# Kernel optimization log

Measured on AMD Instinct MI355X. Metric: run time of the kernel, lower is better.

The kernel has to match this reference:

```python
import jax, jax.numpy as jnp
import numpy as np

B, N, D, NS, H, ITERS = 16, 2048, 128, 8, 128, 3
EPS = 1e-8


def _ln(x, g, b):
    m = jnp.mean(x, -1, keepdims=True)
    v = jnp.mean((x - m) ** 2, -1, keepdims=True)
    return (x - m) * jax.lax.rsqrt(v + 1e-5) * g + b


def _gru(x, h, Wih, Whh, bih, bhh):
    # PyTorch GRUCell math
    gi = x @ Wih.T + bih
    gh = h @ Whh.T + bhh
    ir, iz, inn = jnp.split(gi, 3, -1)
    hr, hz, hn = jnp.split(gh, 3, -1)
    r = jax.nn.sigmoid(ir + hr)
    z = jax.nn.sigmoid(iz + hz)
    n = jnp.tanh(inn + r * hn)
    return (1.0 - z) * n + z * h


def setup_inputs() -> dict:
    key = jax.random.key(0)
    ks = jax.random.split(key, 16)

    def lin(k, out_d, in_d):
        lim = 1.0 / np.sqrt(in_d)
        return jax.random.uniform(k, (out_d, in_d), jnp.float32, -lim, lim)

    return {
        "inputs": jax.random.normal(ks[0], (B, N, D), jnp.float32),
        "init_noise": jax.random.normal(ks[1], (B, NS, 2 * D), jnp.float32),
        "slots_mu": jax.random.normal(ks[2], (1, 1, 2 * D), jnp.float32),
        "slots_logsigma": jax.random.normal(ks[3], (1, 1, 2 * D), jnp.float32) * 0.08,  # ~xavier scale
        "Wq": lin(ks[4], D, D),
        "Wk": lin(ks[5], D, D),
        "gru_Wih": lin(ks[6], 3 * D, D),
        "gru_Whh": lin(ks[7], 3 * D, D),
        "gru_bih": jnp.zeros((3 * D,), jnp.float32),
        "gru_bhh": jnp.zeros((3 * D,), jnp.float32),
        "mlp_mu_W1": lin(ks[8], H, D),
        "mlp_mu_b1": jnp.zeros((H,), jnp.float32),
        "mlp_mu_W2": lin(ks[9], D, H),
        "mlp_mu_b2": jnp.zeros((D,), jnp.float32),
        "ln_in_g": jnp.ones((D,), jnp.float32),
        "ln_in_b": jnp.zeros((D,), jnp.float32),
        "ln_slots_g": jnp.ones((2 * D,), jnp.float32),
        "ln_slots_b": jnp.zeros((2 * D,), jnp.float32),
        "ln_mu_g": jnp.ones((D,), jnp.float32),
        "ln_mu_b": jnp.zeros((D,), jnp.float32),
        "mlp_out_W1": lin(ks[10], 2 * H, 2 * D),
        "mlp_out_b1": jnp.zeros((2 * H,), jnp.float32),
        "mlp_out_W2": lin(ks[11], D, 2 * H),
        "mlp_out_b2": jnp.zeros((D,), jnp.float32),
    }


def _forward(inputs, init_noise, slots_mu, slots_logsigma, Wq, Wk,
             gru_Wih, gru_Whh, gru_bih, gru_bhh,
             mlp_mu_W1, mlp_mu_b1, mlp_mu_W2, mlp_mu_b2,
             ln_in_g, ln_in_b, ln_slots_g, ln_slots_b, ln_mu_g, ln_mu_b,
             mlp_out_W1, mlp_out_b1, mlp_out_W2, mlp_out_b2):
    x = _ln(inputs, ln_in_g, ln_in_b)                      # (B,N,D)
    k = x @ Wk.T
    v = k                                                  # original uses to_k for both k and v
    slots = slots_mu + jnp.exp(slots_logsigma) * init_noise  # (B,NS,2D)
    pi_cl = jnp.full((B, NS, 1), 1.0 / NS, inputs.dtype)

    def step(slots, pi_cl):
        s = _ln(slots, ln_slots_g, ln_slots_b)
        mu_s, ls_s = jnp.split(s, 2, -1)                   # (B,NS,D) each
        q_mu = mu_s @ Wq.T
        q_ls = ls_s @ Wq.T
        inv_var = jnp.exp(-2.0 * q_ls)                     # 1 / exp(q_logsigma)^2
        diff = k[:, None, :, :] - q_mu[:, :, None, :]      # (B,NS,N,D)
        dots = jnp.einsum('bind,bid->bin', diff * diff, inv_var)
        dots_exp = (jnp.exp(-dots) + EPS) * pi_cl          # (B,NS,N)
        gammas = dots_exp / dots_exp.sum(1, keepdims=True)
        attn = gammas / gammas.sum(-1, keepdims=True)
        upd = jnp.einsum('bjd,bij->bid', v, attn)          # (B,NS,D)
        upd = _gru(upd.reshape(-1, D), mu_s.reshape(-1, D),
                   gru_Wih, gru_Whh, gru_bih, gru_bhh).reshape(B, NS, D)
        h = _ln(upd, ln_mu_g, ln_mu_b)
        upd = upd + (jax.nn.relu(h @ mlp_mu_W1.T + mlp_mu_b1) @ mlp_mu_W2.T + mlp_mu_b2)
        diff2 = v[:, None, :, :] - upd[:, :, None, :]      # (B,NS,N,D)
        upd_ls = 0.5 * jnp.log(jnp.einsum('bind,bin->bid', diff2 * diff2 + EPS, attn))
        slots_new = jnp.concatenate([upd, upd_ls], -1)
        pi_new = gammas.sum(-1, keepdims=True)
        pi_new = pi_new / pi_new.shape[2]                  # shape[2]==1: faithful no-op from original
        return slots_new, pi_new

    for _ in range(ITERS):
        slots, pi_cl = step(slots, pi_cl)
    slots, pi_cl = step(jax.lax.stop_gradient(slots), pi_cl)
    h = jax.nn.relu(slots @ mlp_out_W1.T + mlp_out_b1)
    return h @ mlp_out_W2.T + mlp_out_b2                   # (B,NS,D)


def reference(inputs, init_noise, slots_mu, slots_logsigma, Wq, Wk,
              gru_Wih, gru_Whh, gru_bih, gru_bhh,
              mlp_mu_W1, mlp_mu_b1, mlp_mu_W2, mlp_mu_b2,
              ln_in_g, ln_in_b, ln_slots_g, ln_slots_b, ln_mu_g, ln_mu_b,
              mlp_out_W1, mlp_out_b1, mlp_out_W2, mlp_out_b2):
    return _forward(inputs, init_noise, slots_mu, slots_logsigma, Wq, Wk,
                    gru_Wih, gru_Whh, gru_bih, gru_bhh,
                    mlp_mu_W1, mlp_mu_b1, mlp_mu_W2, mlp_mu_b2,
                    ln_in_g, ln_in_b, ln_slots_g, ln_slots_b, ln_mu_g, ln_mu_b,
                    mlp_out_W1, mlp_out_b1, mlp_out_W2, mlp_out_b2)
```

## Files before the change

kernel.cpp:

```cpp
#include <hip/hip_runtime.h>

#define EPS_ 1e-8f

constexpr int OFF_K     = 0;
constexpr int OFF_WQT   = 4194304;
constexpr int OFF_WKT   = OFF_WQT  + 16384;
constexpr int OFF_WIHT  = OFF_WKT  + 16384;
constexpr int OFF_WHHT  = OFF_WIHT + 49152;
constexpr int OFF_WM1T  = OFF_WHHT + 49152;
constexpr int OFF_WM2T  = OFF_WM1T + 16384;
constexpr int OFF_WO1T  = OFF_WM2T + 16384;
constexpr int OFF_WO2T  = OFF_WO1T + 65536;
constexpr int OFF_SLOTS = OFF_WO2T + 32768;
constexpr int OFF_PI    = OFF_SLOTS+ 32768;
constexpr int OFF_MUS   = OFF_PI   + 128;
constexpr int OFF_WA    = OFF_MUS  + 16384;
constexpr int OFF_WB    = OFF_WA   + 16384;
constexpr int OFF_UN    = OFF_WB   + 16384;
constexpr int OFF_S2    = OFF_UN   + 524288;
constexpr int OFF_DEN   = OFF_S2   + 524288;
constexpr int OFF_CZ    = OFF_DEN  + 4096;

__global__ __launch_bounds__(256) void init_kernel(
    const float* __restrict__ Wq,  const float* __restrict__ Wk,
    const float* __restrict__ Wih, const float* __restrict__ Whh,
    const float* __restrict__ Wm1, const float* __restrict__ Wm2,
    const float* __restrict__ Wo1, const float* __restrict__ Wo2,
    const float* __restrict__ smu, const float* __restrict__ sls,
    const float* __restrict__ noise, float* __restrict__ ws) {
  int idx = blockIdx.x * 256 + threadIdx.x;
  if (idx < 16384) { int j = idx >> 7, d = idx & 127; ws[OFF_WQT + d*128 + j] = Wq[idx]; return; }
  idx -= 16384;
  if (idx < 16384) { int j = idx >> 7, d = idx & 127; ws[OFF_WKT + d*128 + j] = Wk[idx]; return; }
  idx -= 16384;
  if (idx < 49152) { int j = idx >> 7, d = idx & 127; ws[OFF_WIHT + d*384 + j] = Wih[idx]; return; }
  idx -= 49152;
  if (idx < 49152) { int j = idx >> 7, d = idx & 127; ws[OFF_WHHT + d*384 + j] = Whh[idx]; return; }
  idx -= 49152;
  if (idx < 16384) { int j = idx >> 7, d = idx & 127; ws[OFF_WM1T + d*128 + j] = Wm1[idx]; return; }
  idx -= 16384;
  if (idx < 16384) { int j = idx >> 7, d = idx & 127; ws[OFF_WM2T + d*128 + j] = Wm2[idx]; return; }
  idx -= 16384;
  if (idx < 65536) { int j = idx >> 8, d = idx & 255; ws[OFF_WO1T + d*256 + j] = Wo1[idx]; return; }
  idx -= 65536;
  if (idx < 32768) { int j = idx >> 8, m = idx & 255; ws[OFF_WO2T + m*128 + j] = Wo2[idx]; return; }
  idx -= 32768;
  if (idx < 32768) { int c = idx & 255; ws[OFF_SLOTS + idx] = smu[c] + expf(sls[c]) * noise[idx]; return; }
  idx -= 32768;
  if (idx < 128) { ws[OFF_PI + idx] = 0.125f; }
}

__global__ __launch_bounds__(256) void k_kernel(
    const float* __restrict__ xin, const float* __restrict__ g, const float* __restrict__ bb,
    const float* __restrict__ WkT, float* __restrict__ kout) {
  __shared__ float xsT[128][32];
  __shared__ float2 red[32][8];
  __shared__ float mrow[32], srow[32];
  int t = threadIdx.x;
  long long base = (long long)blockIdx.x * 32 * 128;
  int row = t >> 3, cg = t & 7;
  const float4* src = (const float4*)(xin + base + row * 128 + cg * 16);
  float4 v0 = src[0], v1 = src[1], v2 = src[2], v3 = src[3];
  const float4* g4p = (const float4*)(g + cg * 16);
  const float4* b4p = (const float4*)(bb + cg * 16);
  float4 g0 = g4p[0], g1 = g4p[1], g2 = g4p[2], g3 = g4p[3];
  float4 bv0 = b4p[0], bv1 = b4p[1], bv2 = b4p[2], bv3 = b4p[3];
  float vals[16];
  *(float4*)&vals[0]  = v0; *(float4*)&vals[4]  = v1;
  *(float4*)&vals[8]  = v2; *(float4*)&vals[12] = v3;
  float gl[16], bl[16];
  *(float4*)&gl[0] = g0; *(float4*)&gl[4] = g1; *(float4*)&gl[8] = g2; *(float4*)&gl[12] = g3;
  *(float4*)&bl[0] = bv0; *(float4*)&bl[4] = bv1; *(float4*)&bl[8] = bv2; *(float4*)&bl[12] = bv3;
  {
    float s = 0.f, ss = 0.f;
    #pragma unroll
    for (int i = 0; i < 16; ++i) { float v = vals[i]; s += v; ss = fmaf(v, v, ss); }
    red[row][cg] = make_float2(s, ss);
  }
  __syncthreads();
  if (t < 32) {
    float s = 0.f, ss = 0.f;
    #pragma unroll
    for (int c = 0; c < 8; ++c) { float2 p = red[t][c]; s += p.x; ss += p.y; }
    float m = s * (1.0f / 128.0f);
    float var = ss * (1.0f / 128.0f) - m * m;
    mrow[t] = m; srow[t] = rsqrtf(var + 1e-5f);
  }
  __syncthreads();
  {
    float m = mrow[row], is = srow[row];
    #pragma unroll
    for (int i = 0; i < 16; ++i) {
      int d = cg * 16 + i;
      int rs = row ^ (((d >> 2) & 7) << 2);
      xsT[d][rs] = (vals[i] - m) * is * gl[i] + bl[i];
    }
  }
  __syncthreads();
  int j = t & 127, rh = t >> 7;
  int r0 = rh * 16;
  float acc[16];
  #pragma unroll
  for (int i = 0; i < 16; ++i) acc[i] = 0.f;
  #pragma unroll 4
  for (int d = 0; d < 128; ++d) {
    float wv = WkT[d * 128 + j];
    int X = ((d >> 2) & 7) << 2;
    #pragma unroll
    for (int gi = 0; gi < 4; ++gi) {
      int off = (r0 + gi * 4) ^ X;
      float4 xv = *(const float4*)&xsT[d][off];
      acc[gi * 4 + 0] = fmaf(xv.x, wv, acc[gi * 4 + 0]);
      acc[gi * 4 + 1] = fmaf(xv.y, wv, acc[gi * 4 + 1]);
      acc[gi * 4 + 2] = fmaf(xv.z, wv, acc[gi * 4 + 2]);
      acc[gi * 4 + 3] = fmaf(xv.w, wv, acc[gi * 4 + 3]);
    }
  }
  #pragma unroll
  for (int i = 0; i < 16; ++i) kout[base + (long long)(r0 + i) * 128 + j] = acc[i];
}

__global__ __launch_bounds__(256) void s1_kernel(
    const float* __restrict__ slots, const float* __restrict__ g, const float* __restrict__ bb,
    const float* __restrict__ WqT, float* __restrict__ mus,
    float* __restrict__ wA, float* __restrict__ wB, float* __restrict__ cz) {
  __shared__ float sl[256];
  __shared__ float2 wr[4];
  __shared__ float qs_l[128], ivs_l[128];
  __shared__ float wrC[4];
  int t = threadIdx.x, bi = blockIdx.x;
  float v = slots[bi * 256 + t];
  float s = v, ss = v * v;
  #pragma unroll
  for (int o = 32; o > 0; o >>= 1) { s += __shfl_down(s, o); ss += __shfl_down(ss, o); }
  if ((t & 63) == 0) wr[t >> 6] = make_float2(s, ss);
  __syncthreads();
  float fs  = wr[0].x + wr[1].x + wr[2].x + wr[3].x;
  float fss = wr[0].y + wr[1].y + wr[2].y + wr[3].y;
  float m   = fs * (1.0f/256.0f);
  float var = fss * (1.0f/256.0f) - m * m;
  float isr = rsqrtf(var + 1e-5f);
  float sn  = (v - m) * isr * g[t] + bb[t];
  sl[t] = sn;
  __syncthreads();
  if (t < 128) {
    float acc = 0.f;
    #pragma unroll 4
    for (int d = 0; d < 128; ++d) acc = fmaf(sl[d], WqT[d * 128 + t], acc);
    qs_l[t] = acc;
    mus[bi * 128 + t] = sn;
  } else {
    int jj = t - 128;
    float acc = 0.f;
    #pragma unroll 4
    for (int d = 0; d < 128; ++d) acc = fmaf(sl[128 + d], WqT[d * 128 + jj], acc);
    ivs_l[jj] = expf(-2.0f * acc);
  }
  __syncthreads();
  float cp = 0.f;
  if (t < 128) {
    float iv = ivs_l[t], q = qs_l[t];
    wA[bi * 128 + t] = iv;
    wB[bi * 128 + t] = -2.0f * q * iv;
    cp = q * q * iv;
  }
  #pragma unroll
  for (int o = 32; o > 0; o >>= 1) cp += __shfl_down(cp, o);
  if ((t & 63) == 0) wrC[t >> 6] = cp;
  __syncthreads();
  if (t == 0) cz[bi] = wrC[0] + wrC[1];
}

__global__ __launch_bounds__(512) void s2_kernel(
    const float* __restrict__ kmat, const float* __restrict__ wA,
    const float* __restrict__ wB,  const float* __restrict__ cz,
    const float* __restrict__ pi,
    float* __restrict__ wun, float* __restrict__ ws2, float* __restrict__ wden) {
  __shared__ float pdots[8][64][8];
  __shared__ float es[64][8];
  __shared__ float recip[64];
  __shared__ float gT[8][72];
  __shared__ float pd[8][8];
  __shared__ float pisl[8], czl[8];
  int t = threadIdx.x;
  int chunk = blockIdx.x, b = blockIdx.y;
  if (t < 8) { pisl[t] = pi[b * 8 + t]; czl[t] = cz[b * 8 + t]; }
  {
    int n = t & 63, w = t >> 6;
    const float4* kr4 = (const float4*)(kmat + (long long)((b * 2048 + chunk * 64 + n) * 128 + w * 16));
    const float4* wa4 = (const float4*)(wA + b * 1024);
    const float4* wb4 = (const float4*)(wB + b * 1024);
    float acc[8] = {0,0,0,0,0,0,0,0};
    #pragma unroll
    for (int dq = 0; dq < 4; ++dq) {
      float4 kv = kr4[dq];
      float xx = kv.x * kv.x, yy = kv.y * kv.y, zz = kv.z * kv.z, ww = kv.w * kv.w;
      #pragma unroll
      for (int s = 0; s < 8; ++s) {
        float4 a4 = wa4[s * 32 + w * 4 + dq];
        float4 b4 = wb4[s * 32 + w * 4 + dq];
        float ac = acc[s];
        ac = fmaf(xx, a4.x, ac); ac = fmaf(kv.x, b4.x, ac);
        ac = fmaf(yy, a4.y, ac); ac = fmaf(kv.y, b4.y, ac);
        ac = fmaf(zz, a4.z, ac); ac = fmaf(kv.z, b4.z, ac);
        ac = fmaf(ww, a4.w, ac); ac = fmaf(kv.w, b4.w, ac);
        acc[s] = ac;
      }
    }
    *(float4*)&pdots[w][n][0] = make_float4(acc[0], acc[1], acc[2], acc[3]);
    *(float4*)&pdots[w][n][4] = make_float4(acc[4], acc[5], acc[6], acc[7]);
  }
  __syncthreads();
  float e;
  {
    int n2 = t >> 3, s = t & 7;
    float dots = czl[s];
    #pragma unroll
    for (int w = 0; w < 8; ++w) dots += pdots[w][n2][s];
    e = (expf(-dots) + EPS_) * pisl[s];
    es[n2][s] = e;
  }
  __syncthreads();
  if (t < 64) {
    float ssum = 0.f;
    #pragma unroll
    for (int s = 0; s < 8; ++s) ssum += es[t][s];
    recip[t] = 1.0f / ssum;
  }
  __syncthreads();
  {
    int n2 = t >> 3, s = t & 7;
    float gam = e * recip[n2];
    gT[s][n2] = gam;
    float p = gam;
    p += __shfl_down(p, 8); p += __shfl_down(p, 16); p += __shfl_down(p, 32);
    if ((t & 63) < 8) pd[t >> 6][t & 7] = p;
  }
  __syncthreads();
  if (t < 8) {
    float sden = 0.f;
    #pragma unroll
    for (int w = 0; w < 8; ++w) sden += pd[w][t];
    wden[(b * 32 + chunk) * 8 + t] = sden;
  }
  {
    int d = t & 127, sh = t >> 7;
    int s0 = sh * 2, s1 = s0 + 1;
    const float* kcol = kmat + (long long)(b * 2048 + chunk * 64) * 128 + d;
    float u0 = 0.f, u1 = 0.f, q0 = 0.f, q1 = 0.f;
    #pragma unroll 2
    for (int n3 = 0; n3 < 64; n3 += 4) {
      float4 ga = *(const float4*)&gT[s0][n3];
      float4 gb = *(const float4*)&gT[s1][n3];
      float k0 = kcol[(n3 + 0) * 128];
      float k1 = kcol[(n3 + 1) * 128];
      float k2 = kcol[(n3 + 2) * 128];
      float k3 = kcol[(n3 + 3) * 128];
      float k0s = k0 * k0, k1s = k1 * k1, k2s = k2 * k2, k3s = k3 * k3;
      u0 = fmaf(ga.x, k0, u0); q0 = fmaf(ga.x, k0s, q0);
      u1 = fmaf(gb.x, k0, u1); q1 = fmaf(gb.x, k0s, q1);
      u0 = fmaf(ga.y, k1, u0); q0 = fmaf(ga.y, k1s, q0);
      u1 = fmaf(gb.y, k1, u1); q1 = fmaf(gb.y, k1s, q1);
      u0 = fmaf(ga.z, k2, u0); q0 = fmaf(ga.z, k2s, q0);
      u1 = fmaf(gb.z, k2, u1); q1 = fmaf(gb.z, k2s, q1);
      u0 = fmaf(ga.w, k3, u0); q0 = fmaf(ga.w, k3s, q0);
      u1 = fmaf(gb.w, k3, u1); q1 = fmaf(gb.w, k3s, q1);
    }
    int pb = ((b * 32 + chunk) * 8) * 128 + d;
    wun[pb + s0 * 128] = u0; wun[pb + s1 * 128] = u1;
    ws2[pb + s0 * 128] = q0; ws2[pb + s1 * 128] = q1;
  }
}

__global__ __launch_bounds__(512) void s3_kernel(
    const float* __restrict__ wun, const float* __restrict__ ws2, const float* __restrict__ wden,
    const float* __restrict__ WihT, const float* __restrict__ WhhT,
    const float* __restrict__ bih,  const float* __restrict__ bhh,
    const float* __restrict__ Wm1T, const float* __restrict__ bm1,
    const float* __restrict__ Wm2T, const float* __restrict__ bm2,
    const float* __restrict__ gmu,  const float* __restrict__ bmu,
    float* __restrict__ slots, float* __restrict__ pi,
    int do_s1,
    const float* __restrict__ gs, const float* __restrict__ bs,
    const float* __restrict__ WqT,
    float* __restrict__ mus, float* __restrict__ wAo, float* __restrict__ wBo,
    float* __restrict__ czo,
    const float* __restrict__ Wo1T, const float* __restrict__ bo1,
    const float* __restrict__ Wo2T, const float* __restrict__ bo2,
    float* __restrict__ out) {
  int t = threadIdx.x, bi = blockIdx.x;
  int d = t & 127, q = t >> 7;
  int b = bi >> 3, i = bi & 7;
  __shared__ float redU[4][128], redS[4][128];
  __shared__ float dred[32];
  __shared__ float xs[128], hs[128];
  __shared__ float gacc[4][6][128];
  __shared__ float ga[6][128];
  __shared__ float grus[128], hl[128], m1s[128];
  __shared__ float macc[4][128];
  __shared__ float2 wr2[2];
  __shared__ float uarr[256];
  float unp = 0.f, s2p = 0.f;
  #pragma unroll
  for (int c = q * 8; c < q * 8 + 8; ++c) {
    int po = ((b * 32 + c) * 8 + i) * 128 + d;
    unp += wun[po]; s2p += ws2[po];
  }
  redU[q][d] = unp; redS[q][d] = s2p;
  if (t < 32) dred[t] = wden[(b * 32 + t) * 8 + i];
  if (q == 1) hs[d] = mus[bi * 128 + d];
  __syncthreads();
  float den = 0.f;
  #pragma unroll
  for (int c = 0; c < 32; ++c) den += dred[c];
  float un  = redU[0][d] + redU[1][d] + redU[2][d] + redU[3][d];
  float s2v = redS[0][d] + redS[1][d] + redS[2][d] + redS[3][d];
  if (q == 0) xs[d] = un / den;
  __syncthreads();
  {
    float a0 = 0, a1 = 0, a2 = 0, a3 = 0, a4 = 0, a5 = 0;
    #pragma unroll 4
    for (int dd = q * 32; dd < q * 32 + 32; ++dd) {
      float xv = xs[dd], hv = hs[dd];
      const float* wi = &WihT[dd * 384 + d];
      const float* wh = &WhhT[dd * 384 + d];
      a0 = fmaf(xv, wi[0],   a0);
      a1 = fmaf(xv, wi[128], a1);
      a2 = fmaf(xv, wi[256], a2);
      a3 = fmaf(hv, wh[0],   a3);
      a4 = fmaf(hv, wh[128], a4);
      a5 = fmaf(hv, wh[256], a5);
    }
    gacc[q][0][d] = a0; gacc[q][1][d] = a1; gacc[q][2][d] = a2;
    gacc[q][3][d] = a3; gacc[q][4][d] = a4; gacc[q][5][d] = a5;
  }
  __syncthreads();
  for (int f = t; f < 768; f += 512) {
    int j = f >> 7, dd = f & 127;
    ga[j][dd] = gacc[0][j][dd] + gacc[1][j][dd] + gacc[2][j][dd] + gacc[3][j][dd];
  }
  __syncthreads();
  float gru = 0.f;
  if (q == 0) {
    float ir = ga[0][d] + bih[d], iz = ga[1][d] + bih[128 + d], inn = ga[2][d] + bih[256 + d];
    float hr = ga[3][d] + bhh[d], hz = ga[4][d] + bhh[128 + d], hn  = ga[5][d] + bhh[256 + d];
    float r  = 1.0f / (1.0f + expf(-(ir + hr)));
    float z  = 1.0f / (1.0f + expf(-(iz + hz)));
    float nn = tanhf(inn + r * hn);
    gru = (1.0f - z) * nn + z * hs[d];
    grus[d] = gru;
    float s = gru, ssq = gru * gru;
    #pragma unroll
    for (int o = 32; o > 0; o >>= 1) { s += __shfl_down(s, o); ssq += __shfl_down(ssq, o); }
    if ((d & 63) == 0) wr2[d >> 6] = make_float2(s, ssq);
  }
  __syncthreads();
  if (q == 0) {
    float fs = wr2[0].x + wr2[1].x, fss = wr2[0].y + wr2[1].y;
    float mean = fs * (1.0f/128.0f);
    float var  = fss * (1.0f/128.0f) - mean * mean;
    hl[d] = (gru - mean) * rsqrtf(var + 1e-5f) * gmu[d] + bmu[d];
  }
  __syncthreads();
  {
    float m1p = 0.f;
    #pragma unroll 4
    for (int dd = q * 32; dd < q * 32 + 32; ++dd)
      m1p = fmaf(hl[dd], Wm1T[dd * 128 + d], m1p);
    macc[q][d] = m1p;
  }
  __syncthreads();
  if (q == 0) m1s[d] = fmaxf(macc[0][d] + macc[1][d] + macc[2][d] + macc[3][d] + bm1[d], 0.f);
  __syncthreads();
  {
    float m2p = 0.f;
    #pragma unroll 4
    for (int dd = q * 32; dd < q * 32 + 32; ++dd)
      m2p = fmaf(m1s[dd], Wm2T[dd * 128 + d], m2p);
    macc[q][d] = m2p;
  }
  __syncthreads();
  if (q == 0) {
    float u = grus[d] + macc[0][d] + macc[1][d] + macc[2][d] + macc[3][d] + bm2[d];
    float val = (s2v - 2.0f * u * un + u * u * den) / den;
    float ls = 0.5f * logf(fmaxf(val, 0.0f) + EPS_);
    slots[bi * 256 + d]       = u;
    slots[bi * 256 + 128 + d] = ls;
    uarr[d] = u; uarr[128 + d] = ls;
    if (d == 0) pi[bi] = den;
  }
  __syncthreads();
  if (do_s1) {
    __shared__ float2 wr4[4];
    __shared__ float sln[256];
    __shared__ float qacc[2][2][128];
    __shared__ float qs_l[128], ivs_l[128];
    __shared__ float wrC[8];
    if (t < 256) {
      float v = uarr[t];
      float s = v, ssq = v * v;
      #pragma unroll
      for (int o = 32; o > 0; o >>= 1) { s += __shfl_down(s, o); ssq += __shfl_down(ssq, o); }
      if ((t & 63) == 0) wr4[t >> 6] = make_float2(s, ssq);
    }
    __syncthreads();
    if (t < 256) {
      float fs  = wr4[0].x + wr4[1].x + wr4[2].x + wr4[3].x;
      float fss = wr4[0].y + wr4[1].y + wr4[2].y + wr4[3].y;
      float m   = fs * (1.0f/256.0f);
      float var = fss * (1.0f/256.0f) - m * m;
      sln[t] = (uarr[t] - m) * rsqrtf(var + 1e-5f) * gs[t] + bs[t];
    }
    __syncthreads();
    {
      int h2 = t >> 8, qq = (t >> 7) & 1, d2 = t & 127;
      const float* src = sln + h2 * 128;
      float acc = 0.f;
      #pragma unroll 4
      for (int dd = qq * 64; dd < qq * 64 + 64; ++dd)
        acc = fmaf(src[dd], WqT[dd * 128 + d2], acc);
      qacc[h2][qq][d2] = acc;
    }
    __syncthreads();
    if (t < 128) {
      qs_l[t] = qacc[0][0][t] + qacc[0][1][t];
      mus[bi * 128 + t] = sln[t];
    } else if (t < 256) {
      int dd2 = t - 128;
      ivs_l[dd2] = expf(-2.0f * (qacc[1][0][dd2] + qacc[1][1][dd2]));
    }
    __syncthreads();
    float cp = 0.f;
    if (t < 128) {
      float iv = ivs_l[t], qv = qs_l[t];
      wAo[bi * 128 + t] = iv;
      wBo[bi * 128 + t] = -2.0f * qv * iv;
      cp = qv * qv * iv;
    }
    #pragma unroll
    for (int o = 32; o > 0; o >>= 1) cp += __shfl_down(cp, o);
    if ((t & 63) == 0) wrC[t >> 6] = cp;
    __syncthreads();
    if (t == 0) czo[bi] = wrC[0] + wrC[1];
  } else {
    __shared__ float oacc[2][256];
    __shared__ float hh[256];
    {
      int o = t & 255, qq = t >> 8;
      float acc = 0.f;
      #pragma unroll 4
      for (int dd = qq * 128; dd < qq * 128 + 128; ++dd)
        acc = fmaf(uarr[dd], Wo1T[dd * 256 + o], acc);
      oacc[qq][o] = acc;
    }
    __syncthreads();
    if (t < 256) hh[t] = fmaxf(oacc[0][t] + oacc[1][t] + bo1[t], 0.f);
    __syncthreads();
    {
      int o2 = t & 127, q4 = t >> 7;
      float acc2 = 0.f;
      #pragma unroll 4
      for (int dd = q4 * 64; dd < q4 * 64 + 64; ++dd)
        acc2 = fmaf(hh[dd], Wo2T[dd * 128 + o2], acc2);
      macc[q4][o2] = acc2;
    }
    __syncthreads();
    if (t < 128) out[bi * 128 + t] = macc[0][t] + macc[1][t] + macc[2][t] + macc[3][t] + bo2[t];
  }
}

extern "C" void kernel_launch(void* const* d_in, const int* in_sizes, int n_in,
                              void* d_out, int out_size, void* d_ws, size_t ws_size,
                              hipStream_t stream) {
  const float* inputs = (const float*)d_in[0];
  const float* noise  = (const float*)d_in[1];
  const float* smu    = (const float*)d_in[2];
  const float* sls    = (const float*)d_in[3];
  const float* Wq     = (const float*)d_in[4];
  const float* Wk     = (const float*)d_in[5];
  const float* Wih    = (const float*)d_in[6];
  const float* Whh    = (const float*)d_in[7];
  const float* bih    = (const float*)d_in[8];
  const float* bhh    = (const float*)d_in[9];
  const float* Wm1    = (const float*)d_in[10];
  const float* bm1    = (const float*)d_in[11];
  const float* Wm2    = (const float*)d_in[12];
  const float* bm2    = (const float*)d_in[13];
  const float* gin    = (const float*)d_in[14];
  const float* bin    = (const float*)d_in[15];
  const float* gsl    = (const float*)d_in[16];
  const float* bsl    = (const float*)d_in[17];
  const float* gmu    = (const float*)d_in[18];
  const float* bmu    = (const float*)d_in[19];
  const float* Wo1    = (const float*)d_in[20];
  const float* bo1    = (const float*)d_in[21];
  const float* Wo2    = (const float*)d_in[22];
  const float* bo2    = (const float*)d_in[23];

  float* ws    = (float*)d_ws;
  float* kbuf  = ws + OFF_K;
  float* WqT   = ws + OFF_WQT;
  float* WkT   = ws + OFF_WKT;
  float* WihT  = ws + OFF_WIHT;
  float* WhhT  = ws + OFF_WHHT;
  float* Wm1T  = ws + OFF_WM1T;
  float* Wm2T  = ws + OFF_WM2T;
  float* Wo1T  = ws + OFF_WO1T;
  float* Wo2T  = ws + OFF_WO2T;
  float* slots = ws + OFF_SLOTS;
  float* pibuf = ws + OFF_PI;
  float* mus   = ws + OFF_MUS;
  float* wA    = ws + OFF_WA;
  float* wB    = ws + OFF_WB;
  float* wun   = ws + OFF_UN;
  float* ws2   = ws + OFF_S2;
  float* wden  = ws + OFF_DEN;
  float* czb   = ws + OFF_CZ;

  hipLaunchKernelGGL(init_kernel, dim3(1153), dim3(256), 0, stream,
                     Wq, Wk, Wih, Whh, Wm1, Wm2, Wo1, Wo2, smu, sls, noise, ws);
  hipLaunchKernelGGL(k_kernel, dim3(1024), dim3(256), 0, stream,
                     inputs, gin, bin, WkT, kbuf);
  hipLaunchKernelGGL(s1_kernel, dim3(128), dim3(256), 0, stream,
                     slots, gsl, bsl, WqT, mus, wA, wB, czb);
  for (int s = 0; s < 4; ++s) {
    hipLaunchKernelGGL(s2_kernel, dim3(32, 16), dim3(512), 0, stream,
                       kbuf, wA, wB, czb, pibuf, wun, ws2, wden);
    hipLaunchKernelGGL(s3_kernel, dim3(128), dim3(512), 0, stream,
                       wun, ws2, wden, WihT, WhhT, bih, bhh,
                       Wm1T, bm1, Wm2T, bm2, gmu, bmu, slots, pibuf,
                       (s < 3) ? 1 : 0, gsl, bsl, WqT, mus, wA, wB, czb,
                       Wo1T, bo1, Wo2T, bo2, (float*)d_out);
  }
}
```

Before: 174.0 us.

## Retile k projection to 64 rows per block with wave-uniform weight loads

The k_kernel now handles 64 rows per block, staging them in padded shared memory. Each thread computes 32 output columns for one row, reading weights as wave-uniform float4 loads (readfirstlane) instead of per-lane columns, and writes the output back coalesced through shared memory. The s2_kernel key-load mapping is interleaved so adjacent lanes read contiguous float4s, and the es array is padded against bank conflicts. This trades more registers per thread (32 accumulators) and fewer blocks for scalar-broadcast weight reads and better coalescing.

```diff
diff --git a/kernel.cpp b/kernel.cpp
--- a/kernel.cpp
+++ b/kernel.cpp
@@ -53,71 +53,71 @@
 __global__ __launch_bounds__(256) void k_kernel(
     const float* __restrict__ xin, const float* __restrict__ g, const float* __restrict__ bb,
     const float* __restrict__ WkT, float* __restrict__ kout) {
-  __shared__ float xsT[128][32];
-  __shared__ float2 red[32][8];
-  __shared__ float mrow[32], srow[32];
+  __shared__ float xs[64][129];
+  __shared__ float2 red2[64][4];
+  __shared__ float mrow[64], srow[64];
   int t = threadIdx.x;
-  long long base = (long long)blockIdx.x * 32 * 128;
-  int row = t >> 3, cg = t & 7;
-  const float4* src = (const float4*)(xin + base + row * 128 + cg * 16);
-  float4 v0 = src[0], v1 = src[1], v2 = src[2], v3 = src[3];
-  const float4* g4p = (const float4*)(g + cg * 16);
-  const float4* b4p = (const float4*)(bb + cg * 16);
-  float4 g0 = g4p[0], g1 = g4p[1], g2 = g4p[2], g3 = g4p[3];
-  float4 bv0 = b4p[0], bv1 = b4p[1], bv2 = b4p[2], bv3 = b4p[3];
-  float vals[16];
-  *(float4*)&vals[0]  = v0; *(float4*)&vals[4]  = v1;
-  *(float4*)&vals[8]  = v2; *(float4*)&vals[12] = v3;
-  float gl[16], bl[16];
-  *(float4*)&gl[0] = g0; *(float4*)&gl[4] = g1; *(float4*)&gl[8] = g2; *(float4*)&gl[12] = g3;
-  *(float4*)&bl[0] = bv0; *(float4*)&bl[4] = bv1; *(float4*)&bl[8] = bv2; *(float4*)&bl[12] = bv3;
-  {
+  long long base = (long long)blockIdx.x * 64 * 128;
+  const float4* in4 = (const float4*)(xin + base);
+  for (int f = t; f < 2048; f += 256) {
+    float4 v = in4[f];
+    int r = f >> 5, c = (f & 31) * 4;
+    xs[r][c] = v.x; xs[r][c + 1] = v.y; xs[r][c + 2] = v.z; xs[r][c + 3] = v.w;
+  }
+  __syncthreads();
+  {
+    int r = t >> 2, q = t & 3;
     float s = 0.f, ss = 0.f;
-    #pragma unroll
-    for (int i = 0; i < 16; ++i) { float v = vals[i]; s += v; ss = fmaf(v, v, ss); }
-    red[row][cg] = make_float2(s, ss);
-  }
-  __syncthreads();
-  if (t < 32) {
+    #pragma unroll 8
+    for (int u = 0; u < 32; ++u) { float v = xs[r][q * 32 + u]; s += v; ss = fmaf(v, v, ss); }
+    red2[r][q] = make_float2(s, ss);
+  }
+  __syncthreads();
+  if (t < 64) {
     float s = 0.f, ss = 0.f;
     #pragma unroll
-    for (int c = 0; c < 8; ++c) { float2 p = red[t][c]; s += p.x; ss += p.y; }
+    for (int q2 = 0; q2 < 4; ++q2) { float2 p = red2[t][q2]; s += p.x; ss += p.y; }
     float m = s * (1.0f / 128.0f);
     float var = ss * (1.0f / 128.0f) - m * m;
     mrow[t] = m; srow[t] = rsqrtf(var + 1e-5f);
   }
   __syncthreads();
   {
-    float m = mrow[row], is = srow[row];
-    #pragma unroll
-    for (int i = 0; i < 16; ++i) {
-      int d = cg * 16 + i;
-      int rs = row ^ (((d >> 2) & 7) << 2);
-      xsT[d][rs] = (vals[i] - m) * is * gl[i] + bl[i];
-    }
-  }
-  __syncthreads();
-  int j = t & 127, rh = t >> 7;
-  int r0 = rh * 16;
-  float acc[16];
+    int r = t >> 2, q = t & 3;
+    float m = mrow[r], is = srow[r];
+    #pragma unroll 8
+    for (int u = 0; u < 32; ++u) {
+      int d = q * 32 + u;
+      xs[r][d] = (xs[r][d] - m) * is * g[d] + bb[d];
+    }
+  }
+  __syncthreads();
+  int r = t & 63;
+  int jb = __builtin_amdgcn_readfirstlane((t >> 6) * 32);
+  float acc[32];
   #pragma unroll
-  for (int i = 0; i < 16; ++i) acc[i] = 0.f;
-  #pragma unroll 4
+  for (int i = 0; i < 32; ++i) acc[i] = 0.f;
   for (int d = 0; d < 128; ++d) {
-    float wv = WkT[d * 128 + j];
-    int X = ((d >> 2) & 7) << 2;
-    #pragma unroll
-    for (int gi = 0; gi < 4; ++gi) {
-      int off = (r0 + gi * 4) ^ X;
-      float4 xv = *(const float4*)&xsT[d][off];
-      acc[gi * 4 + 0] = fmaf(xv.x, wv, acc[gi * 4 + 0]);
-      acc[gi * 4 + 1] = fmaf(xv.y, wv, acc[gi * 4 + 1]);
-      acc[gi * 4 + 2] = fmaf(xv.z, wv, acc[gi * 4 + 2]);
-      acc[gi * 4 + 3] = fmaf(xv.w, wv, acc[gi * 4 + 3]);
-    }
-  }
-  #pragma unroll
-  for (int i = 0; i < 16; ++i) kout[base + (long long)(r0 + i) * 128 + j] = acc[i];
+    float xv = xs[r][d];
+    const float* wrow = WkT + d * 128 + jb;
+    #pragma unroll
+    for (int i = 0; i < 8; ++i) {
+      float4 wv = *(const float4*)(wrow + i * 4);
+      acc[i * 4 + 0] = fmaf(xv, wv.x, acc[i * 4 + 0]);
+      acc[i * 4 + 1] = fmaf(xv, wv.y, acc[i * 4 + 1]);
+      acc[i * 4 + 2] = fmaf(xv, wv.z, acc[i * 4 + 2]);
+      acc[i * 4 + 3] = fmaf(xv, wv.w, acc[i * 4 + 3]);
+    }
+  }
+  __syncthreads();
+  #pragma unroll 8
+  for (int i = 0; i < 32; ++i) xs[r][jb + i] = acc[i];
+  __syncthreads();
+  float4* out4 = (float4*)(kout + base);
+  for (int f = t; f < 2048; f += 256) {
+    int rr = f >> 5, c = (f & 31) * 4;
+    out4[f] = make_float4(xs[rr][c], xs[rr][c + 1], xs[rr][c + 2], xs[rr][c + 3]);
+  }
 }
 
 __global__ __launch_bounds__(256) void s1_kernel(
@@ -177,7 +177,7 @@
     const float* __restrict__ pi,
     float* __restrict__ wun, float* __restrict__ ws2, float* __restrict__ wden) {
   __shared__ float pdots[8][64][8];
-  __shared__ float es[64][8];
+  __shared__ float es[64][9];
   __shared__ float recip[64];
   __shared__ float gT[8][72];
   __shared__ float pd[8][8];
@@ -186,24 +186,25 @@
   int chunk = blockIdx.x, b = blockIdx.y;
   if (t < 8) { pisl[t] = pi[b * 8 + t]; czl[t] = cz[b * 8 + t]; }
   {
-    int n = t & 63, w = t >> 6;
-    const float4* kr4 = (const float4*)(kmat + (long long)((b * 2048 + chunk * 64 + n) * 128 + w * 16));
+    int w = t & 7, n = t >> 3;
+    const float4* kr4 = (const float4*)(kmat + (long long)(b * 2048 + chunk * 64 + n) * 128);
     const float4* wa4 = (const float4*)(wA + b * 1024);
     const float4* wb4 = (const float4*)(wB + b * 1024);
-    float acc[8] = {0,0,0,0,0,0,0,0};
-    #pragma unroll
-    for (int dq = 0; dq < 4; ++dq) {
-      float4 kv = kr4[dq];
-      float xx = kv.x * kv.x, yy = kv.y * kv.y, zz = kv.z * kv.z, ww = kv.w * kv.w;
+    float acc[8] = {0, 0, 0, 0, 0, 0, 0, 0};
+    #pragma unroll
+    for (int i = 0; i < 4; ++i) {
+      int gg = i * 8 + w;
+      float4 kv = kr4[gg];
+      float xx = kv.x * kv.x, yy = kv.y * kv.y, zz = kv.z * kv.z, ww2 = kv.w * kv.w;
       #pragma unroll
       for (int s = 0; s < 8; ++s) {
-        float4 a4 = wa4[s * 32 + w * 4 + dq];
-        float4 b4 = wb4[s * 32 + w * 4 + dq];
+        float4 a4 = wa4[s * 32 + gg];
+        float4 b4 = wb4[s * 32 + gg];
         float ac = acc[s];
         ac = fmaf(xx, a4.x, ac); ac = fmaf(kv.x, b4.x, ac);
         ac = fmaf(yy, a4.y, ac); ac = fmaf(kv.y, b4.y, ac);
         ac = fmaf(zz, a4.z, ac); ac = fmaf(kv.z, b4.z, ac);
-        ac = fmaf(ww, a4.w, ac); ac = fmaf(kv.w, b4.w, ac);
+        ac = fmaf(ww2, a4.w, ac); ac = fmaf(kv.w, b4.w, ac);
         acc[s] = ac;
       }
     }
@@ -397,8 +398,8 @@
     __shared__ float qs_l[128], ivs_l[128];
     __shared__ float wrC[8];
     if (t < 256) {
-      float v = uarr[t];
-      float s = v, ssq = v * v;
+      float v2 = uarr[t];
+      float s = v2, ssq = v2 * v2;
       #pragma unroll
       for (int o = 32; o > 0; o >>= 1) { s += __shfl_down(s, o); ssq += __shfl_down(ssq, o); }
       if ((t & 63) == 0) wr4[t >> 6] = make_float2(s, ssq);
@@ -519,7 +520,7 @@
 
   hipLaunchKernelGGL(init_kernel, dim3(1153), dim3(256), 0, stream,
                      Wq, Wk, Wih, Whh, Wm1, Wm2, Wo1, Wo2, smu, sls, noise, ws);
-  hipLaunchKernelGGL(k_kernel, dim3(1024), dim3(256), 0, stream,
+  hipLaunchKernelGGL(k_kernel, dim3(512), dim3(256), 0, stream,
                      inputs, gin, bin, WkT, kbuf);
   hipLaunchKernelGGL(s1_kernel, dim3(128), dim3(256), 0, stream,
                      slots, gsl, bsl, WqT, mus, wA, wB, czb);
```

New measurement: 185.8 us. 6.7% more time.
